# Kernel optimization log

Measured on AMD Instinct MI355X. Metric: run time of the kernel, lower is better.

## Reference

```python
import jax, jax.numpy as jnp
import numpy as np

B, H, D, V = 1024, 4, 128, 100000
EPS = 1e-7  # keras backend epsilon used by SparseCategoricalCrossentropy clipping


def setup_inputs() -> dict:
    key = jax.random.key(0)
    k0, k1, k2, k3, k4 = jax.random.split(key, 5)
    inputs = jax.random.normal(k0, (B, D), dtype=jnp.float32)
    label = jax.random.randint(k1, (B,), 0, V)
    embeddings = jax.random.normal(k2, (V, D), dtype=jnp.float32) * 0.05
    proj_mat = jax.random.normal(k3, (H * D, D), dtype=jnp.float32) * 0.05
    mix_mat = jax.random.normal(k4, (H, D), dtype=jnp.float32) * 0.05
    return {"inputs": inputs, "label": label, "embeddings": embeddings,
            "proj_mat": proj_mat, "mix_mat": mix_mat}


def reference(inputs, label, embeddings, proj_mat, mix_mat):
    # proj: [B, H*D] -> [B, H, D] with tanh nonlinearity
    proj = jnp.tanh(inputs @ proj_mat.T).reshape(-1, H, D)
    # mixture weights pi: [B, H]
    pi = jax.nn.softmax(inputs @ mix_mat.T, axis=-1)
    # per-head full-vocab logits/probs: [B, H, V]
    head_logits = jnp.einsum('bhd,vd->bhv', proj, embeddings)
    head_probs = jax.nn.softmax(head_logits, axis=-1)
    # mixture of softmaxes: [B, V]
    probs = jnp.einsum('bh,bhv->bv', pi, head_probs)
    # sparse categorical cross-entropy on probabilities (not logits)
    p_label = jnp.take_along_axis(probs, label[:, None], axis=1)[:, 0]
    loss = -jnp.mean(jnp.log(jnp.clip(p_label, EPS, 1.0)))
    return probs, loss
```

## Files before the change

kernel.cpp:

```cpp
#include <hip/hip_runtime.h>
#include <math.h>

#define B_ 1024
#define H_ 4
#define D_ 128
#define V_ 100000
#define M_ (B_*H_)
#define EPS_ 1e-7f
#define LOG2E_ 1.4426950408889634f

#define VT_ 64
#define NT_ 1563
#define YB_ 16
#define TPB_ 98

typedef unsigned short ushort_t;
typedef __attribute__((ext_vector_type(4))) float f32x4;
typedef __attribute__((ext_vector_type(8))) short bf16x8;

__device__ __forceinline__ ushort_t f2bf(float f) {
    unsigned u = __float_as_uint(f);
    unsigned r = u + 0x7fffu + ((u >> 16) & 1u);
    return (ushort_t)(r >> 16);
}

__device__ __forceinline__ void gload_lds16(const void* g, void* l) {
    __builtin_amdgcn_global_load_lds(
        (const __attribute__((address_space(1))) unsigned int*)g,
        (__attribute__((address_space(3))) unsigned int*)l,
        16, 0, 0);
}

__global__ __launch_bounds__(512)
void proj_pi_kernel(const float* __restrict__ inputs, const float* __restrict__ proj_mat,
                    const float* __restrict__ mix_mat, ushort_t* __restrict__ Abf,
                    float* __restrict__ pi)
{
    __shared__ float xin[128];
    __shared__ float mixv[4];
    const int b = blockIdx.x, tid = threadIdx.x;
    if (tid < 128) xin[tid] = inputs[b * 128 + tid];
    __syncthreads();

    const float4* row = (const float4*)(proj_mat + tid * 128);
    float acc = 0.f;
#pragma unroll 8
    for (int k = 0; k < 32; ++k) {
        float4 m4 = row[k];
        acc += m4.x * xin[k*4+0] + m4.y * xin[k*4+1] + m4.z * xin[k*4+2] + m4.w * xin[k*4+3];
    }
    Abf[b * 512 + tid] = f2bf(LOG2E_ * tanhf(acc));

    if (tid < 4) {
        const float4* mrow = (const float4*)(mix_mat + tid * 128);
        float a2 = 0.f;
#pragma unroll 8
        for (int k = 0; k < 32; ++k) {
            float4 m4 = mrow[k];
            a2 += m4.x * xin[k*4+0] + m4.y * xin[k*4+1] + m4.z * xin[k*4+2] + m4.w * xin[k*4+3];
        }
        mixv[tid] = a2;
    }
    __syncthreads();
    if (tid < 4) {
        float m = fmaxf(fmaxf(mixv[0], mixv[1]), fmaxf(mixv[2], mixv[3]));
        float e0 = __expf(mixv[0]-m), e1 = __expf(mixv[1]-m), e2 = __expf(mixv[2]-m), e3 = __expf(mixv[3]-m);
        float s = e0 + e1 + e2 + e3;
        float mye = __expf(mixv[tid]-m);
        pi[b * 4 + tid] = mye / s;
    }
}

__global__ __launch_bounds__(256)
void conv_kernel(const float* __restrict__ e, ushort_t* __restrict__ o, int n4)
{
    int i = blockIdx.x * 256 + threadIdx.x;
    if (i < n4) {
        float4 f = ((const float4*)e)[i];
        ushort4 u;
        u.x = f2bf(f.x); u.y = f2bf(f.y); u.z = f2bf(f.z); u.w = f2bf(f.w);
        ((ushort4*)o)[i] = u;
    }
}

__device__ __forceinline__ void stage_a(const ushort_t* __restrict__ Abf, ushort_t* lds_a,
                                        int m0, int tid, int wave)
{
#pragma unroll
    for (int t = 0; t < 8; ++t) {
        int r  = t * 16 + (tid >> 4);
        int c  = tid & 15;
        int cs = c ^ (r & 7);
        unsigned loff = (unsigned)__builtin_amdgcn_readfirstlane(t * 4096 + wave * 1024);
        gload_lds16(Abf + (size_t)(m0 + r) * 128 + cs * 8, (char*)lds_a + loff);
    }
}

__device__ __forceinline__ void stage_e(const ushort_t* __restrict__ Ebf, ushort_t* ldsb,
                                        int v0, int tid, int wave)
{
#pragma unroll
    for (int t = 0; t < 4; ++t) {
        int r  = t * 16 + (tid >> 4);
        int c  = tid & 15;
        int cs = c ^ (r & 7);
        int vrow = v0 + r; if (vrow >= V_) vrow = V_ - 1;
        unsigned loff = (unsigned)__builtin_amdgcn_readfirstlane(t * 4096 + wave * 1024);
        gload_lds16(Ebf + (size_t)vrow * 128 + cs * 8, (char*)ldsb + loff);
    }
}

template <int PASS>
__global__ __launch_bounds__(256, 2)
void gemm_kernel(const ushort_t* __restrict__ Abf, const ushort_t* __restrict__ Ebf,
                 const float* __restrict__ pi, float* __restrict__ Z,
                 float* __restrict__ probs)
{
    __shared__ ushort_t lds_a[128 * 128];
    __shared__ ushort_t lds_e[2][64 * 128];
    __shared__ float w_lds[128];

    const int tid  = threadIdx.x;
    const int wave = tid >> 6;
    const int lane = tid & 63;
    const int q    = lane >> 4;
    const int r16  = lane & 15;
    const int m0   = blockIdx.x * 128;
    const int wm   = (wave >> 1) * 64;
    const int wn   = (wave & 1) * 32;

    const int t_begin = blockIdx.y * TPB_;
    int t_end = t_begin + TPB_; if (t_end > NT_) t_end = NT_;

    if (PASS == 2 && tid < 128) {
        int gi = m0 + tid;
        w_lds[tid] = pi[gi] / Z[gi];
    }

    stage_a(Abf, lds_a, m0, tid, wave);
    stage_e(Ebf, lds_e[0], t_begin * VT_, tid, wave);
    __syncthreads();

    float wreg[4][4];
    if (PASS == 2) {
#pragma unroll
        for (int mi = 0; mi < 4; ++mi)
#pragma unroll
            for (int j = 0; j < 4; ++j)
                wreg[mi][j] = w_lds[wm + mi * 16 + q * 4 + j];
    }

    float zs[4][4];
    if (PASS == 1) {
#pragma unroll
        for (int mi = 0; mi < 4; ++mi)
#pragma unroll
            for (int h = 0; h < 4; ++h) zs[mi][h] = 0.f;
    }

    int bb = 0;
    for (int vt = t_begin; vt < t_end; ++vt) {
        if (vt + 1 < t_end)
            stage_e(Ebf, lds_e[bb ^ 1], (vt + 1) * VT_, tid, wave);

        f32x4 acc[4][2];
#pragma unroll
        for (int mi = 0; mi < 4; ++mi)
#pragma unroll
            for (int ni = 0; ni < 2; ++ni) acc[mi][ni] = (f32x4)(0.f);

#pragma unroll
        for (int kk = 0; kk < 4; ++kk) {
            int chunk = kk * 4 + q;
            bf16x8 fa[4], fb[2];
#pragma unroll
            for (int mi = 0; mi < 4; ++mi) {
                int row = wm + mi * 16 + r16;
                int sc  = chunk ^ (row & 7);
                fa[mi] = *(const bf16x8*)&lds_a[row * 128 + sc * 8];
            }
#pragma unroll
            for (int ni = 0; ni < 2; ++ni) {
                int row = wn + ni * 16 + r16;
                int sc  = chunk ^ (row & 7);
                fb[ni] = *(const bf16x8*)&lds_e[bb][row * 128 + sc * 8];
            }
#pragma unroll
            for (int mi = 0; mi < 4; ++mi)
#pragma unroll
                for (int ni = 0; ni < 2; ++ni)
                    acc[mi][ni] = __builtin_amdgcn_mfma_f32_16x16x32_bf16(fa[mi], fb[ni], acc[mi][ni], 0, 0, 0);
        }

        __syncthreads();

        if (PASS == 1) {
#pragma unroll
            for (int mi = 0; mi < 4; ++mi)
#pragma unroll
                for (int ni = 0; ni < 2; ++ni) {
                    int v = vt * VT_ + wn + ni * 16 + r16;
                    bool ok = (v < V_);
#pragma unroll
                    for (int h = 0; h < 4; ++h) {
                        float e = exp2f(acc[mi][ni][h]);
                        zs[mi][h] += ok ? e : 0.f;
                    }
                }
        } else {
#pragma unroll
            for (int mi = 0; mi < 4; ++mi) {
                int mloc = wm + mi * 16 + q * 4;
                size_t rowoff = (size_t)((m0 + mloc) >> 2) * V_;
#pragma unroll
                for (int ni = 0; ni < 2; ++ni) {
                    int v = vt * VT_ + wn + ni * 16 + r16;
                    if (v < V_) {
                        f32x4 a = acc[mi][ni];
                        float p = wreg[mi][0] * exp2f(a[0]) + wreg[mi][1] * exp2f(a[1])
                                + wreg[mi][2] * exp2f(a[2]) + wreg[mi][3] * exp2f(a[3]);
                        probs[rowoff + v] = p;
                    }
                }
            }
        }
        bb ^= 1;
    }

    if (PASS == 1) {
#pragma unroll
        for (int msk = 1; msk < 16; msk <<= 1) {
#pragma unroll
            for (int mi = 0; mi < 4; ++mi)
#pragma unroll
                for (int h = 0; h < 4; ++h)
                    zs[mi][h] += __shfl_xor(zs[mi][h], msk, 64);
        }
        int mi = r16 >> 2, h = r16 & 3;
        int midx = m0 + wm + mi * 16 + q * 4 + h;
        atomicAdd(&Z[midx], zs[mi][h]);
    }
}

__global__ __launch_bounds__(256)
void loss_kernel(const float* __restrict__ probs, const int* __restrict__ label,
                 float* __restrict__ out)
{
    __shared__ float red[256];
    int tid = threadIdx.x;
    float s = 0.f;
    for (int b = tid; b < B_; b += 256) {
        float p = probs[(size_t)b * V_ + label[b]];
        p = fminf(fmaxf(p, EPS_), 1.0f);
        s -= logf(p);
    }
    red[tid] = s;
    __syncthreads();
    for (int st = 128; st > 0; st >>= 1) {
        if (tid < st) red[tid] += red[tid + st];
        __syncthreads();
    }
    if (tid == 0) out[0] = red[0] / (float)B_;
}

extern "C" void kernel_launch(void* const* d_in, const int* in_sizes, int n_in,
                              void* d_out, int out_size, void* d_ws, size_t ws_size,
                              hipStream_t stream)
{
    const float* inputs   = (const float*)d_in[0];
    const int*   label    = (const int*)d_in[1];
    const float* emb      = (const float*)d_in[2];
    const float* proj_mat = (const float*)d_in[3];
    const float* mix_mat  = (const float*)d_in[4];
    float* out = (float*)d_out;

    char* ws = (char*)d_ws;
    ushort_t* emb_bf = (ushort_t*)ws;
    ushort_t* A_bf   = (ushort_t*)(ws + 25600000);
    float*    pi     = (float*)(ws + 26648576);
    float*    Z      = (float*)(ws + 26664960);

    conv_kernel<<<12500, 256, 0, stream>>>(emb, emb_bf, 3200000);
    proj_pi_kernel<<<1024, 512, 0, stream>>>(inputs, proj_mat, mix_mat, A_bf, pi);
    hipMemsetAsync(Z, 0, 4096 * sizeof(float), stream);

    dim3 g(32, YB_);
    gemm_kernel<1><<<g, 256, 0, stream>>>(A_bf, emb_bf, nullptr, Z, nullptr);
    gemm_kernel<2><<<g, 256, 0, stream>>>(A_bf, emb_bf, pi, Z, out);

    loss_kernel<<<1, 256, 0, stream>>>(out, label, out + (size_t)B_ * V_);
}
```

Before: 840.8 us.

## Keep A fragments in registers and switch to 32x32x16 MFMA with 128-wide vocab tiles

Removes the LDS staging of the A (projected activations) tile and loads each wave's A fragments straight into registers once, where they stay for the whole vocab sweep. Switches from 16x16x32 to 32x32x16 bf16 MFMA, doubles the vocab tile to 128 rows with a wider XOR swizzle, and rewrites the epilogue and the Z reduction for the 32x32 accumulator layout. The aim is to cut LDS reads per MFMA and raise arithmetic intensity. In exchange it uses far more registers (64 VGPRs of A fragments plus 64 accumulators), which may lower occupancy below the two-blocks-per-SM launch bound.

```diff
diff --git a/kernel.cpp b/kernel.cpp
--- a/kernel.cpp
+++ b/kernel.cpp
@@ -9,13 +9,14 @@
 #define EPS_ 1e-7f
 #define LOG2E_ 1.4426950408889634f
 
-#define VT_ 64
-#define NT_ 1563
+#define VT_ 128
+#define NT_ 782
 #define YB_ 16
-#define TPB_ 98
+#define TPB_ 49
 
 typedef unsigned short ushort_t;
 typedef __attribute__((ext_vector_type(4))) float f32x4;
+typedef __attribute__((ext_vector_type(16))) float f32x16;
 typedef __attribute__((ext_vector_type(8))) short bf16x8;
 
 __device__ __forceinline__ ushort_t f2bf(float f) {
@@ -83,27 +84,14 @@
     }
 }
 
-__device__ __forceinline__ void stage_a(const ushort_t* __restrict__ Abf, ushort_t* lds_a,
-                                        int m0, int tid, int wave)
+__device__ __forceinline__ void stage_e(const ushort_t* __restrict__ Ebf, ushort_t* ldsb,
+                                        int v0, int tid, int wave)
 {
 #pragma unroll
     for (int t = 0; t < 8; ++t) {
         int r  = t * 16 + (tid >> 4);
         int c  = tid & 15;
-        int cs = c ^ (r & 7);
-        unsigned loff = (unsigned)__builtin_amdgcn_readfirstlane(t * 4096 + wave * 1024);
-        gload_lds16(Abf + (size_t)(m0 + r) * 128 + cs * 8, (char*)lds_a + loff);
-    }
-}
-
-__device__ __forceinline__ void stage_e(const ushort_t* __restrict__ Ebf, ushort_t* ldsb,
-                                        int v0, int tid, int wave)
-{
-#pragma unroll
-    for (int t = 0; t < 4; ++t) {
-        int r  = t * 16 + (tid >> 4);
-        int c  = tid & 15;
-        int cs = c ^ (r & 7);
+        int cs = c ^ (r & 15);
         int vrow = v0 + r; if (vrow >= V_) vrow = V_ - 1;
         unsigned loff = (unsigned)__builtin_amdgcn_readfirstlane(t * 4096 + wave * 1024);
         gload_lds16(Ebf + (size_t)vrow * 128 + cs * 8, (char*)ldsb + loff);
@@ -116,18 +104,17 @@
                  const float* __restrict__ pi, float* __restrict__ Z,
                  float* __restrict__ probs)
 {
-    __shared__ ushort_t lds_a[128 * 128];
-    __shared__ ushort_t lds_e[2][64 * 128];
+    __shared__ ushort_t lds_e[2][VT_ * 128];
     __shared__ float w_lds[128];
 
     const int tid  = threadIdx.x;
     const int wave = tid >> 6;
     const int lane = tid & 63;
-    const int q    = lane >> 4;
-    const int r16  = lane & 15;
+    const int l31  = lane & 31;
+    const int hi   = lane >> 5;
     const int m0   = blockIdx.x * 128;
     const int wm   = (wave >> 1) * 64;
-    const int wn   = (wave & 1) * 32;
+    const int wn   = (wave & 1) * 64;
 
     const int t_begin = blockIdx.y * TPB_;
     int t_end = t_begin + TPB_; if (t_end > NT_) t_end = NT_;
@@ -137,25 +124,33 @@
         w_lds[tid] = pi[gi] / Z[gi];
     }
 
-    stage_a(Abf, lds_a, m0, tid, wave);
+    bf16x8 fa[2][8];
+#pragma unroll
+    for (int mi = 0; mi < 2; ++mi) {
+        const ushort_t* arow = Abf + (size_t)(m0 + wm + mi * 32 + l31) * 128 + hi * 8;
+#pragma unroll
+        for (int kk = 0; kk < 8; ++kk)
+            fa[mi][kk] = *(const bf16x8*)(arow + kk * 16);
+    }
+
     stage_e(Ebf, lds_e[0], t_begin * VT_, tid, wave);
     __syncthreads();
 
-    float wreg[4][4];
+    f32x4 wq[2][4];
     if (PASS == 2) {
 #pragma unroll
-        for (int mi = 0; mi < 4; ++mi)
-#pragma unroll
-            for (int j = 0; j < 4; ++j)
-                wreg[mi][j] = w_lds[wm + mi * 16 + q * 4 + j];
-    }
-
-    float zs[4][4];
+        for (int mi = 0; mi < 2; ++mi)
+#pragma unroll
+            for (int g = 0; g < 4; ++g)
+                wq[mi][g] = *(const f32x4*)&w_lds[wm + mi * 32 + g * 8 + hi * 4];
+    }
+
+    float zs[2][16];
     if (PASS == 1) {
 #pragma unroll
-        for (int mi = 0; mi < 4; ++mi)
-#pragma unroll
-            for (int h = 0; h < 4; ++h) zs[mi][h] = 0.f;
+        for (int mi = 0; mi < 2; ++mi)
+#pragma unroll
+            for (int r = 0; r < 16; ++r) zs[mi][r] = 0.f;
     }
 
     int bb = 0;
@@ -163,82 +158,81 @@
         if (vt + 1 < t_end)
             stage_e(Ebf, lds_e[bb ^ 1], (vt + 1) * VT_, tid, wave);
 
-        f32x4 acc[4][2];
-#pragma unroll
-        for (int mi = 0; mi < 4; ++mi)
-#pragma unroll
-            for (int ni = 0; ni < 2; ++ni) acc[mi][ni] = (f32x4)(0.f);
-
-#pragma unroll
-        for (int kk = 0; kk < 4; ++kk) {
-            int chunk = kk * 4 + q;
-            bf16x8 fa[4], fb[2];
-#pragma unroll
-            for (int mi = 0; mi < 4; ++mi) {
-                int row = wm + mi * 16 + r16;
-                int sc  = chunk ^ (row & 7);
-                fa[mi] = *(const bf16x8*)&lds_a[row * 128 + sc * 8];
-            }
+        f32x16 acc[2][2];
+#pragma unroll
+        for (int mi = 0; mi < 2; ++mi)
+#pragma unroll
+            for (int ni = 0; ni < 2; ++ni) acc[mi][ni] = (f32x16)(0.f);
+
+#pragma unroll
+        for (int kk = 0; kk < 8; ++kk) {
+            bf16x8 fb[2];
 #pragma unroll
             for (int ni = 0; ni < 2; ++ni) {
-                int row = wn + ni * 16 + r16;
-                int sc  = chunk ^ (row & 7);
+                int row = wn + ni * 32 + l31;
+                int sc  = (kk * 2 + hi) ^ (row & 15);
                 fb[ni] = *(const bf16x8*)&lds_e[bb][row * 128 + sc * 8];
             }
 #pragma unroll
-            for (int mi = 0; mi < 4; ++mi)
+            for (int mi = 0; mi < 2; ++mi)
 #pragma unroll
                 for (int ni = 0; ni < 2; ++ni)
-                    acc[mi][ni] = __builtin_amdgcn_mfma_f32_16x16x32_bf16(fa[mi], fb[ni], acc[mi][ni], 0, 0, 0);
+                    acc[mi][ni] = __builtin_amdgcn_mfma_f32_32x32x16_bf16(
+                        fa[mi][kk], fb[ni], acc[mi][ni], 0, 0, 0);
         }
 
         __syncthreads();
 
+        const int vbase = vt * VT_ + wn + l31;
         if (PASS == 1) {
-#pragma unroll
-            for (int mi = 0; mi < 4; ++mi)
-#pragma unroll
-                for (int ni = 0; ni < 2; ++ni) {
-                    int v = vt * VT_ + wn + ni * 16 + r16;
-                    bool ok = (v < V_);
-#pragma unroll
-                    for (int h = 0; h < 4; ++h) {
-                        float e = exp2f(acc[mi][ni][h]);
-                        zs[mi][h] += ok ? e : 0.f;
+            bool ok0 = (vbase < V_), ok1 = (vbase + 32 < V_);
+#pragma unroll
+            for (int mi = 0; mi < 2; ++mi)
+#pragma unroll
+                for (int r = 0; r < 16; ++r) {
+                    float e0 = ok0 ? exp2f(acc[mi][0][r]) : 0.f;
+                    float e1 = ok1 ? exp2f(acc[mi][1][r]) : 0.f;
+                    zs[mi][r] += e0 + e1;
+                }
+        } else {
+#pragma unroll
+            for (int mi = 0; mi < 2; ++mi)
+#pragma unroll
+                for (int g = 0; g < 4; ++g) {
+                    size_t rowoff = (size_t)((m0 + wm + mi * 32 + g * 8 + hi * 4) >> 2) * V_;
+#pragma unroll
+                    for (int ni = 0; ni < 2; ++ni) {
+                        int v = vbase + ni * 32;
+                        if (v < V_) {
+                            float p = wq[mi][g].x * exp2f(acc[mi][ni][4*g+0])
+                                    + wq[mi][g].y * exp2f(acc[mi][ni][4*g+1])
+                                    + wq[mi][g].z * exp2f(acc[mi][ni][4*g+2])
+                                    + wq[mi][g].w * exp2f(acc[mi][ni][4*g+3]);
+                            probs[rowoff + v] = p;
+                        }
                     }
                 }
-        } else {
-#pragma unroll
-            for (int mi = 0; mi < 4; ++mi) {
-                int mloc = wm + mi * 16 + q * 4;
-                size_t rowoff = (size_t)((m0 + mloc) >> 2) * V_;
-#pragma unroll
-                for (int ni = 0; ni < 2; ++ni) {
-                    int v = vt * VT_ + wn + ni * 16 + r16;
-                    if (v < V_) {
-                        f32x4 a = acc[mi][ni];
-                        float p = wreg[mi][0] * exp2f(a[0]) + wreg[mi][1] * exp2f(a[1])
-                                + wreg[mi][2] * exp2f(a[2]) + wreg[mi][3] * exp2f(a[3]);
-                        probs[rowoff + v] = p;
-                    }
+        }
+        bb ^= 1;
+    }
+
+    if (PASS == 1) {
+#pragma unroll
+        for (int msk = 1; msk < 32; msk <<= 1)
+#pragma unroll
+            for (int mi = 0; mi < 2; ++mi)
+#pragma unroll
+                for (int r = 0; r < 16; ++r)
+                    zs[mi][r] += __shfl_xor(zs[mi][r], msk, 64);
+#pragma unroll
+        for (int mi = 0; mi < 2; ++mi)
+#pragma unroll
+            for (int r = 0; r < 16; ++r) {
+                if (l31 == mi * 16 + r) {
+                    int m = m0 + wm + mi * 32 + (r & 3) + 8 * (r >> 2) + 4 * hi;
+                    atomicAdd(&Z[m], zs[mi][r]);
                 }
             }
-        }
-        bb ^= 1;
-    }
-
-    if (PASS == 1) {
-#pragma unroll
-        for (int msk = 1; msk < 16; msk <<= 1) {
-#pragma unroll
-            for (int mi = 0; mi < 4; ++mi)
-#pragma unroll
-                for (int h = 0; h < 4; ++h)
-                    zs[mi][h] += __shfl_xor(zs[mi][h], msk, 64);
-        }
-        int mi = r16 >> 2, h = r16 & 3;
-        int midx = m0 + wm + mi * 16 + q * 4 + h;
-        atomicAdd(&Z[midx], zs[mi][h]);
     }
 }
 
```

Measured after the change: 758.3 us. 1.11x faster.
